# Performance work log

Hardware: AMD Instinct MI355X
Metric: run time of the kernel (lower is better)

Reference implementation:

```python
import jax, jax.numpy as jnp
import numpy as np

IN_SIZE = 1024
OUT_SIZE = 3 * IN_SIZE  # must equal 3*in_size for trigger_a * attn broadcast
B, S = 32, 512


def setup_inputs() -> dict:
    key = jax.random.key(0)
    ks = jax.random.split(key, 8)
    h_state = jax.random.normal(ks[0], (B, S, 2 * IN_SIZE), dtype=jnp.float32)
    x = jax.random.normal(ks[1], (B, S, IN_SIZE), dtype=jnp.float32)
    trigger = jax.random.randint(ks[2], (B,), 0, S)
    mask = jax.random.randint(ks[3], (B, S), 0, 2).astype(jnp.int32)
    # learned params (nn.Linear: y = x @ W.T + b; store pre-transposed as (in, out))
    Wa = jax.random.normal(ks[4], (3 * IN_SIZE, OUT_SIZE), dtype=jnp.float32) / np.sqrt(3 * IN_SIZE)
    ba = jnp.zeros((OUT_SIZE,), dtype=jnp.float32)
    Ws = jax.random.normal(ks[5], (2 * IN_SIZE, OUT_SIZE), dtype=jnp.float32) / np.sqrt(2 * IN_SIZE)
    bs = jnp.zeros((OUT_SIZE,), dtype=jnp.float32)
    return {"h_state": h_state, "x": x, "trigger": trigger, "mask": mask,
            "Wa": Wa, "ba": ba, "Ws": Ws, "bs": bs}


def reference(h_state, x, trigger, mask, Wa, ba, Ws, bs):
    # a: (B, S, 3*in_size)
    a = jnp.concatenate([h_state, x], axis=-1)
    b = a.shape[0]
    # one_hot + masked_select in the original == gather of the trigger row per batch
    trigger_a = a[jnp.arange(b), trigger]  # (B, 3*in_size)
    s = h_state.sum(axis=1)  # (B, 2*in_size)
    # et: (B, S, out_size)
    et = jnp.tanh(a @ Wa + ba + (s @ Ws + bs)[:, None, :])
    # masked_fill where mask == 0 (mask broadcast over feature dim)
    et = jnp.where(mask[:, :, None] == 0, jnp.float32(-1e9), et)
    # softmax over the FEATURE dim (dim=-1), as in the original; dropout in eval mode is identity
    attn = jax.nn.softmax(et, axis=-1)
    # trigger-weighted reduction over the sequence dim
    out = (trigger_a[:, None, :] * attn).sum(axis=1)  # (B, out_size)
    return out
```

## Files before the change

kernel.cpp:

```cpp
#include <hip/hip_runtime.h>
#include <hip/hip_bf16.h>
#include <hip/hip_fp16.h>


namespace {
constexpr int SIN  = 1024;
constexpr int KH   = 2048;
constexpr int NF   = 3072;
constexpr int NBAT = 32;
constexpr int NS   = 512;
constexpr int NM   = NBAT * NS;
constexpr int NDB  = NF / 64;
constexpr int KC   = 8;
constexpr int NKT  = NF / 64;
}

typedef unsigned short u16;
typedef __bf16 bf16x8 __attribute__((ext_vector_type(8)));
typedef float  f32x4  __attribute__((ext_vector_type(4)));

#define ASYNC_CP16(gptr, lptr)                                                              \
  __builtin_amdgcn_global_load_lds((__attribute__((address_space(1))) void*)(gptr),         \
                                   (__attribute__((address_space(3))) void*)(lptr), 16, 0, 0)

__device__ __forceinline__ u16 f2b(float f) {
  union { float f; unsigned u; } v; v.f = f;
  unsigned u = v.u;
  u += 0x7FFFu + ((u >> 16) & 1u);
  return (u16)(u >> 16);
}

__global__ __launch_bounds__(64) void k_cnt(const int* __restrict__ mask,
                                            int* __restrict__ bcnt) {
  int b = blockIdx.x, t = threadIdx.x;
  int c = 0;
#pragma unroll
  for (int i = 0; i < NS / 64; ++i) c += mask[b * NS + i * 64 + t];
#pragma unroll
  for (int off = 32; off >= 1; off >>= 1) c += __shfl_down(c, off, 64);
  if (t == 0) bcnt[b] = c;
}

__global__ __launch_bounds__(64) void k_scan(const int* __restrict__ bcnt,
                                             int* __restrict__ boff,
                                             int* __restrict__ meta) {
  if (threadIdx.x == 0) {
    int run = 0;
    for (int b = 0; b < NBAT; ++b) { boff[b] = run; run += bcnt[b]; }
    meta[0] = run;
    meta[1] = (run + 255) & ~255;
  }
}

__global__ __launch_bounds__(512) void k_gather(const int* __restrict__ mask,
                                                const int* __restrict__ boff,
                                                const int* __restrict__ meta,
                                                int* __restrict__ rowmap) {
  __shared__ int ps[NS];
  int b = blockIdx.x, t = threadIdx.x;
  int m = mask[b * NS + t];
  ps[t] = m;
  __syncthreads();
#pragma unroll
  for (int off = 1; off < NS; off <<= 1) {
    int v = (t >= off) ? ps[t - off] : 0;
    __syncthreads();
    ps[t] += v;
    __syncthreads();
  }
  if (m) rowmap[boff[b] + ps[t] - m] = b * NS + t;
  if (b == 0) {
    int Mc = meta[0], McPad = meta[1];
    if (Mc + t < McPad) rowmap[Mc + t] = 0;
  }
}

__global__ __launch_bounds__(256) void k_sum_h(const float* __restrict__ h,
                                               float* __restrict__ s) {
  int b = blockIdx.x;
  int d = blockIdx.y * 256 + threadIdx.x;
  const float* p = h + (size_t)b * NS * KH + d;
  float acc = 0.f;
#pragma unroll 8
  for (int t = 0; t < NS; ++t) acc += p[(size_t)t * KH];
  s[b * KH + d] = acc;
}

__global__ __launch_bounds__(256) void k_base1(const float* __restrict__ s,
                                               const float* __restrict__ Ws,
                                               float* __restrict__ basep) {
  __shared__ float sT[NBAT][KH / KC];
  int f  = blockIdx.x * 256 + threadIdx.x;
  int k0 = blockIdx.y * (KH / KC);
  for (int it = 0; it < NBAT; ++it) {
    int idx = it * 256 + threadIdx.x;
    int b = idx >> 8, kk = idx & 255;
    sT[b][kk] = s[b * KH + k0 + kk];
  }
  __syncthreads();
  float acc[NBAT] = {};
  for (int k = 0; k < KH / KC; ++k) {
    float w = Ws[(size_t)(k0 + k) * NF + f];
#pragma unroll
    for (int b = 0; b < NBAT; ++b) acc[b] += sT[b][k] * w;
  }
#pragma unroll
  for (int b = 0; b < NBAT; ++b)
    basep[((size_t)blockIdx.y * NBAT + b) * NF + f] = acc[b];
}

__global__ __launch_bounds__(256) void k_base2(const float* __restrict__ basep,
                                               const float* __restrict__ ba,
                                               const float* __restrict__ bs,
                                               float* __restrict__ base) {
  int b = blockIdx.x;
  int f = blockIdx.y * 256 + threadIdx.x;
  float acc = 0.f;
#pragma unroll
  for (int kc = 0; kc < KC; ++kc) acc += basep[((size_t)kc * NBAT + b) * NF + f];
  base[b * NF + f] = acc + ba[f] + bs[f];
}

__global__ __launch_bounds__(256) void k_cvt_a(const float* __restrict__ h,
                                               const float* __restrict__ x,
                                               const int* __restrict__ rowmap,
                                               const int* __restrict__ meta,
                                               u16* __restrict__ A) {
  int tid = blockIdx.x * 256 + threadIdx.x;
  int i = tid / (NF / 4);
  if (i >= meta[1]) return;
  int k = (tid - i * (NF / 4)) * 4;
  ushort4 o;
  if (i >= meta[0]) {
    o.x = o.y = o.z = o.w = 0;
  } else {
    int ro = rowmap[i];
    int b = ro >> 9, t = ro & 511;
    const float* src = (k < KH) ? h + ((size_t)b * NS + t) * KH + k
                                : x + ((size_t)b * NS + t) * SIN + (k - KH);
    float4 v = *(const float4*)src;
    o.x = f2b(v.x); o.y = f2b(v.y); o.z = f2b(v.z); o.w = f2b(v.w);
  }
  *(ushort4*)(A + (size_t)i * NF + k) = o;
}

__global__ __launch_bounds__(256) void k_wat(const float* __restrict__ Wa,
                                             u16* __restrict__ WaT) {
  __shared__ float tile[64][65];
  int k0 = blockIdx.x * 64, f0 = blockIdx.y * 64;
  int tid = threadIdx.x;
  int col4 = (tid & 15) * 4, row = tid >> 4;
#pragma unroll
  for (int rr = 0; rr < 64; rr += 16) {
    float4 v = *(const float4*)(Wa + (size_t)(k0 + row + rr) * NF + f0 + col4);
    tile[row + rr][col4 + 0] = v.x; tile[row + rr][col4 + 1] = v.y;
    tile[row + rr][col4 + 2] = v.z; tile[row + rr][col4 + 3] = v.w;
  }
  __syncthreads();
#pragma unroll
  for (int rr = 0; rr < 64; rr += 16) {
    int f = f0 + row + rr;
    ushort4 o;
    o.x = f2b(tile[col4 + 0][row + rr]); o.y = f2b(tile[col4 + 1][row + rr]);
    o.z = f2b(tile[col4 + 2][row + rr]); o.w = f2b(tile[col4 + 3][row + rr]);
    *(ushort4*)(WaT + (size_t)f * NF + k0 + col4) = o;
  }
}

#define LDSOFF(row, gg) ((row) * 32 + ((((gg) ^ (((row) >> 1) & 3))) << 3))

#define LDB4(BUF, KS)                                                        \
  _Pragma("unroll") for (int nf = 0; nf < 4; ++nf) {                         \
    int rb = wc * 64 + nf * 16 + lr;                                         \
    bfr[nf] = *(const bf16x8*)&lds[BUF][1][KS][LDSOFF(rb, g)];               \
  }

#define LDA4(BUF, KS, MH)                                                    \
  _Pragma("unroll") for (int mf = 0; mf < 4; ++mf) {                         \
    int ra = wr * 128 + ((MH) * 4 + mf) * 16 + lr;                           \
    afr[mf] = *(const bf16x8*)&lds[BUF][0][KS][LDSOFF(ra, g)];               \
  }

#define MFMA16(MH)                                                           \
  _Pragma("unroll") for (int mf = 0; mf < 4; ++mf)                           \
  _Pragma("unroll") for (int nf = 0; nf < 4; ++nf)                           \
    acc[(MH) * 4 + mf][nf] = __builtin_amdgcn_mfma_f32_16x16x32_bf16(        \
        afr[mf], bfr[nf], acc[(MH) * 4 + mf][nf], 0, 0, 0);

#define STAGE(SMAT, SBUF, SKS, SKT)                                          \
  if ((SKT) < NKT) {                                                         \
    _Pragma("unroll") for (int q = 0; q < 2; ++q) {                          \
      const u16* src = ((SMAT) ? pB[q] : pA[q]) + (SKT) * 64 + (SKS) * 32;   \
      ASYNC_CP16(src, &lds[SBUF][SMAT][SKS][q * 4096 + wid * 512]);          \
    }                                                                        \
  }

#define PH(BUF, KS, MH, SMAT, SBUF, SKS, SKT, VM)                            \
  {                                                                          \
    if ((MH) == 0) { LDB4(BUF, KS) }                                         \
    LDA4(BUF, KS, MH)                                                        \
    STAGE(SMAT, SBUF, SKS, SKT)                                              \
    __builtin_amdgcn_s_barrier();                                            \
    asm volatile("s_waitcnt lgkmcnt(0)" ::: "memory");                       \
    __builtin_amdgcn_s_setprio(1);                                           \
    MFMA16(MH)                                                               \
    __builtin_amdgcn_s_setprio(0);                                           \
    if (VM) asm volatile("s_waitcnt vmcnt(4)" ::: "memory");                 \
    __builtin_amdgcn_s_barrier();                                            \
  }

__global__ __launch_bounds__(512, 2) void k_gemm(const u16* __restrict__ A,
                                                 const u16* __restrict__ Wt,
                                                 const float* __restrict__ base,
                                                 const int* __restrict__ rowmap,
                                                 const int* __restrict__ meta,
                                                 __half* __restrict__ P,
                                                 float* __restrict__ Dpart) {
  __shared__ __align__(16) u16 lds[2][2][2][8192];
  const int MT   = meta[1] >> 8;
  const int nact = MT * 12;
  const int flat = blockIdx.x;
  if (flat >= nact) return;
  const int qx = nact >> 3, rx = nact & 7;
  const int xcd = flat & 7, idx = flat >> 3;
  const int swz = (xcd < rx) ? xcd * (qx + 1) + idx
                             : rx * (qx + 1) + (xcd - rx) * qx + idx;
  const int mt = swz / 12, nt = swz - mt * 12;
  const int r0 = mt << 8, c0 = nt << 8;

  const int tid = threadIdx.x;
  const int wid = tid >> 6, lane = tid & 63;
  const int wr = wid >> 2, wc = wid & 3;
  const int g = lane >> 4, lr = lane & 15;

  const u16* pA[2]; const u16* pB[2];
#pragma unroll
  for (int q = 0; q < 2; ++q) {
    int c = q * 512 + tid;
    int row = c >> 2;
    int kc8 = (((c & 3) ^ ((row >> 1) & 3)) << 3);
    pA[q] = A  + (size_t)(r0 + row) * NF + kc8;
    pB[q] = Wt + (size_t)(c0 + row) * NF + kc8;
  }

  f32x4 acc[8][4] = {};
  bf16x8 afr[4], bfr[4];

  STAGE(0, 0, 0, 0) STAGE(1, 0, 0, 0)
  STAGE(0, 0, 1, 0) STAGE(1, 0, 1, 0)
  STAGE(0, 1, 0, 1) STAGE(1, 1, 0, 1)
  asm volatile("s_waitcnt vmcnt(4)" ::: "memory");
  __builtin_amdgcn_s_barrier();

#pragma unroll 1
  for (int i = 0; i < NKT / 2; ++i) {
    const int kt1 = 2 * i + 1, kt2 = 2 * i + 2, kt3 = 2 * i + 3;
    PH(0, 0, 0, 0, 1, 1, kt1, 0)
    PH(0, 0, 1, 1, 1, 1, kt1, 0)
    PH(0, 1, 0, 0, 0, 0, kt2, 0)
    PH(0, 1, 1, 1, 0, 0, kt2, 1)
    PH(1, 0, 0, 0, 0, 1, kt2, 0)
    PH(1, 0, 1, 1, 0, 1, kt2, 0)
    PH(1, 1, 0, 0, 1, 0, kt3, 0)
    PH(1, 1, 1, 1, 1, 0, kt3, 1)
  }

  const int cbase = c0 + wc * 64;
#pragma unroll
  for (int mf = 0; mf < 8; ++mf) {
#pragma unroll
    for (int j = 0; j < 4; ++j) {
      int i = r0 + wr * 128 + mf * 16 + g * 4 + j;
      int b = rowmap[i] >> 9;
      float rs = 0.f;
#pragma unroll
      for (int nf = 0; nf < 4; ++nf) {
        int ccn = cbase + nf * 16 + lr;
        float z  = acc[mf][nf][j] + base[b * NF + ccn];
        z        = fminf(fmaxf(z, -15.f), 15.f);
        float e2 = __expf(2.f * z);
        float th = (e2 - 1.f) / (e2 + 1.f);
        float p  = __expf(th);
        P[(size_t)i * NF + ccn] = __float2half(p);
        rs += p;
      }
#pragma unroll
      for (int off = 1; off < 16; off <<= 1) rs += __shfl_xor(rs, off, 64);
      if (lr == 0) Dpart[(size_t)i * NDB + (cbase >> 6)] = rs;
    }
  }
}

__global__ __launch_bounds__(256) void k_invd(const float* __restrict__ Dpart,
                                              const int* __restrict__ meta,
                                              float* __restrict__ invD) {
  int i = blockIdx.x * 256 + threadIdx.x;
  if (i >= meta[1]) return;
  float d = 0.f;
#pragma unroll
  for (int q = 0; q < NDB; ++q) d += Dpart[(size_t)i * NDB + q];
  invD[i] = 1.0f / d;
}

__global__ __launch_bounds__(384) void k_final(const __half* __restrict__ P,
                                               const float* __restrict__ invD,
                                               const int* __restrict__ boff,
                                               const int* __restrict__ bcnt,
                                               const float* __restrict__ h,
                                               const float* __restrict__ x,
                                               const int* __restrict__ trig,
                                               float* __restrict__ out) {
  int b = blockIdx.x;
  int f0 = threadIdx.x * 8;
  int off = boff[b], cnt = bcnt[b];
  const __half* Pp = P + (size_t)off * NF + f0;
  const float*  iv = invD + off;
  float acc[8] = {};
  for (int t = 0; t < cnt; ++t) {
    int4 v = *(const int4*)(Pp + (size_t)t * NF);
    float ivt = iv[t];
    const __half2* h2 = (const __half2*)&v;
#pragma unroll
    for (int k = 0; k < 4; ++k) {
      float2 f2 = __half22float2(h2[k]);
      acc[2 * k]     += f2.x * ivt;
      acc[2 * k + 1] += f2.y * ivt;
    }
  }
  float uni = (float)(NS - cnt) * (1.0f / (float)NF);
  int tr = trig[b];
#pragma unroll
  for (int k = 0; k < 8; ++k) {
    int f = f0 + k;
    float ta = (f < KH) ? h[((size_t)b * NS + tr) * KH + f]
                        : x[((size_t)b * NS + tr) * SIN + f - KH];
    out[b * NF + f] = (acc[k] + uni) * ta;
  }
}

extern "C" void kernel_launch(void* const* d_in, const int* in_sizes, int n_in,
                              void* d_out, int out_size, void* d_ws, size_t ws_size,
                              hipStream_t stream) {
  const float* h_state = (const float*)d_in[0];
  const float* x       = (const float*)d_in[1];
  const int*   trigger = (const int*)d_in[2];
  const int*   mask    = (const int*)d_in[3];
  const float* Wa      = (const float*)d_in[4];
  const float* ba      = (const float*)d_in[5];
  const float* Ws      = (const float*)d_in[6];
  const float* bs      = (const float*)d_in[7];
  float*       out     = (float*)d_out;

  char* w = (char*)d_ws;
  u16*    Abf   = (u16*)w;                 w += (size_t)NM * NF * 2;
  u16*    WaT   = (u16*)w;                 w += (size_t)NF * NF * 2;
  __half* P     = (__half*)w;              w += (size_t)NM * NF * 2;
  float*  s     = (float*)w;               w += (size_t)NBAT * KH * 4;
  float*  base  = (float*)w;               w += (size_t)NBAT * NF * 4;
  float*  Dpart = (float*)w;               w += (size_t)NM * NDB * 4;
  float*  basep = (float*)Dpart;
  float*  invD  = (float*)w;               w += (size_t)NM * 4;
  int*    rowmap= (int*)w;                 w += (size_t)NM * 4;
  int*    bcnt  = (int*)w;                 w += 128;
  int*    boff  = (int*)w;                 w += 128;
  int*    meta  = (int*)w;                 w += 128;

  (void)in_sizes; (void)n_in; (void)out_size; (void)ws_size;

  k_cnt   <<<dim3(NBAT), 64, 0, stream>>>(mask, bcnt);
  k_scan  <<<dim3(1), 64, 0, stream>>>(bcnt, boff, meta);
  k_gather<<<dim3(NBAT), 512, 0, stream>>>(mask, boff, meta, rowmap);
  k_sum_h <<<dim3(NBAT, KH / 256), 256, 0, stream>>>(h_state, s);
  k_cvt_a <<<dim3(NM * (NF / 4) / 256), 256, 0, stream>>>(h_state, x, rowmap, meta, Abf);
  k_wat   <<<dim3(NF / 64, NF / 64), 256, 0, stream>>>(Wa, WaT);
  k_base1 <<<dim3(NF / 256, KC), 256, 0, stream>>>(s, Ws, basep);
  k_base2 <<<dim3(NBAT, NF / 256), 256, 0, stream>>>(basep, ba, bs, base);
  k_gemm  <<<dim3((NF / 256) * (NM / 256)), 512, 0, stream>>>(Abf, WaT, base, rowmap, meta, P, Dpart);
  k_invd  <<<dim3(NM / 256), 256, 0, stream>>>(Dpart, meta, invD);
  k_final <<<dim3(NBAT), 384, 0, stream>>>(P, invD, boff, bcnt, h_state, x, trigger, out);
}
```

Measured before the change: 464.8 us.

## Split final reduction across sequence chunks and relax GEMM vmcnt waits

The final weighted sum over the sequence, which ran as only 32 blocks, becomes a two-stage reduction. The first stage uses 8 sequence chunks per batch across feature tiles and writes partial sums into a reused workspace; the second stage sums the partials and applies the trigger scaling. Separately, the GEMM pipeline drops the conditional vmcnt(4) waits and waits on vmcnt(6) in every phase, with vmcnt(8) in the prologue, to keep more async loads in flight. The wait change risks a race if the count no longer covers the stage about to be read. The first reduction stage also uses scalar half loads, which are less efficient than the previous vectorized loads.

```diff
diff --git a/kernel.cpp b/kernel.cpp
--- a/kernel.cpp
+++ b/kernel.cpp
@@ -13,6 +13,7 @@
 constexpr int NDB  = NF / 64;
 constexpr int KC   = 8;
 constexpr int NKT  = NF / 64;
+constexpr int NCH  = 8;
 }
 
 typedef unsigned short u16;
@@ -195,7 +196,7 @@
     }                                                                        \
   }
 
-#define PH(BUF, KS, MH, SMAT, SBUF, SKS, SKT, VM)                            \
+#define PH(BUF, KS, MH, SMAT, SBUF, SKS, SKT)                                \
   {                                                                          \
     if ((MH) == 0) { LDB4(BUF, KS) }                                         \
     LDA4(BUF, KS, MH)                                                        \
@@ -205,7 +206,7 @@
     __builtin_amdgcn_s_setprio(1);                                           \
     MFMA16(MH)                                                               \
     __builtin_amdgcn_s_setprio(0);                                           \
-    if (VM) asm volatile("s_waitcnt vmcnt(4)" ::: "memory");                 \
+    asm volatile("s_waitcnt vmcnt(6)" ::: "memory");                         \
     __builtin_amdgcn_s_barrier();                                            \
   }
 
@@ -249,20 +250,20 @@
   STAGE(0, 0, 0, 0) STAGE(1, 0, 0, 0)
   STAGE(0, 0, 1, 0) STAGE(1, 0, 1, 0)
   STAGE(0, 1, 0, 1) STAGE(1, 1, 0, 1)
-  asm volatile("s_waitcnt vmcnt(4)" ::: "memory");
+  asm volatile("s_waitcnt vmcnt(8)" ::: "memory");
   __builtin_amdgcn_s_barrier();
 
 #pragma unroll 1
   for (int i = 0; i < NKT / 2; ++i) {
     const int kt1 = 2 * i + 1, kt2 = 2 * i + 2, kt3 = 2 * i + 3;
-    PH(0, 0, 0, 0, 1, 1, kt1, 0)
-    PH(0, 0, 1, 1, 1, 1, kt1, 0)
-    PH(0, 1, 0, 0, 0, 0, kt2, 0)
-    PH(0, 1, 1, 1, 0, 0, kt2, 1)
-    PH(1, 0, 0, 0, 0, 1, kt2, 0)
-    PH(1, 0, 1, 1, 0, 1, kt2, 0)
-    PH(1, 1, 0, 0, 1, 0, kt3, 0)
-    PH(1, 1, 1, 1, 1, 0, kt3, 1)
+    PH(0, 0, 0, 0, 1, 1, kt1)
+    PH(0, 0, 1, 1, 1, 1, kt1)
+    PH(0, 1, 0, 0, 0, 0, kt2)
+    PH(0, 1, 1, 1, 0, 0, kt2)
+    PH(1, 0, 0, 0, 0, 1, kt2)
+    PH(1, 0, 1, 1, 0, 1, kt2)
+    PH(1, 1, 0, 0, 1, 0, kt3)
+    PH(1, 1, 1, 1, 1, 0, kt3)
   }
 
   const int cbase = c0 + wc * 64;
@@ -302,40 +303,39 @@
   invD[i] = 1.0f / d;
 }
 
-__global__ __launch_bounds__(384) void k_final(const __half* __restrict__ P,
-                                               const float* __restrict__ invD,
-                                               const int* __restrict__ boff,
-                                               const int* __restrict__ bcnt,
-                                               const float* __restrict__ h,
-                                               const float* __restrict__ x,
-                                               const int* __restrict__ trig,
-                                               float* __restrict__ out) {
+__global__ __launch_bounds__(256) void k_final1(const __half* __restrict__ P,
+                                                const float* __restrict__ invD,
+                                                const int* __restrict__ boff,
+                                                const int* __restrict__ bcnt,
+                                                float* __restrict__ pb) {
+  int c = blockIdx.x;
+  int b = c >> 3, j = c & 7;
+  int f = blockIdx.y * 256 + threadIdx.x;
+  int cnt = bcnt[b];
+  int lo = j * 64, hi = min(cnt, lo + 64);
+  int off = boff[b];
+  float acc = 0.f;
+  for (int t = lo; t < hi; ++t)
+    acc += __half2float(P[(size_t)(off + t) * NF + f]) * invD[off + t];
+  pb[(size_t)c * NF + f] = acc;
+}
+
+__global__ __launch_bounds__(256) void k_final2(const float* __restrict__ pb,
+                                                const int* __restrict__ bcnt,
+                                                const float* __restrict__ h,
+                                                const float* __restrict__ x,
+                                                const int* __restrict__ trig,
+                                                float* __restrict__ out) {
   int b = blockIdx.x;
-  int f0 = threadIdx.x * 8;
-  int off = boff[b], cnt = bcnt[b];
-  const __half* Pp = P + (size_t)off * NF + f0;
-  const float*  iv = invD + off;
-  float acc[8] = {};
-  for (int t = 0; t < cnt; ++t) {
-    int4 v = *(const int4*)(Pp + (size_t)t * NF);
-    float ivt = iv[t];
-    const __half2* h2 = (const __half2*)&v;
-#pragma unroll
-    for (int k = 0; k < 4; ++k) {
-      float2 f2 = __half22float2(h2[k]);
-      acc[2 * k]     += f2.x * ivt;
-      acc[2 * k + 1] += f2.y * ivt;
-    }
-  }
-  float uni = (float)(NS - cnt) * (1.0f / (float)NF);
+  int f = blockIdx.y * 256 + threadIdx.x;
+  float acc = 0.f;
+#pragma unroll
+  for (int j = 0; j < NCH; ++j) acc += pb[(size_t)(b * NCH + j) * NF + f];
+  acc += (float)(NS - bcnt[b]) * (1.0f / (float)NF);
   int tr = trig[b];
-#pragma unroll
-  for (int k = 0; k < 8; ++k) {
-    int f = f0 + k;
-    float ta = (f < KH) ? h[((size_t)b * NS + tr) * KH + f]
-                        : x[((size_t)b * NS + tr) * SIN + f - KH];
-    out[b * NF + f] = (acc[k] + uni) * ta;
-  }
+  float ta = (f < KH) ? h[((size_t)b * NS + tr) * KH + f]
+                      : x[((size_t)b * NS + tr) * SIN + f - KH];
+  out[b * NF + f] = acc * ta;
 }
 
 extern "C" void kernel_launch(void* const* d_in, const int* in_sizes, int n_in,
@@ -359,6 +359,7 @@
   float*  base  = (float*)w;               w += (size_t)NBAT * NF * 4;
   float*  Dpart = (float*)w;               w += (size_t)NM * NDB * 4;
   float*  basep = (float*)Dpart;
+  float*  pb    = (float*)Dpart;
   float*  invD  = (float*)w;               w += (size_t)NM * 4;
   int*    rowmap= (int*)w;                 w += (size_t)NM * 4;
   int*    bcnt  = (int*)w;                 w += 128;
@@ -377,5 +378,6 @@
   k_base2 <<<dim3(NBAT, NF / 256), 256, 0, stream>>>(basep, ba, bs, base);
   k_gemm  <<<dim3((NF / 256) * (NM / 256)), 512, 0, stream>>>(Abf, WaT, base, rowmap, meta, P, Dpart);
   k_invd  <<<dim3(NM / 256), 256, 0, stream>>>(Dpart, meta, invD);
-  k_final <<<dim3(NBAT), 384, 0, stream>>>(P, invD, boff, bcnt, h_state, x, trigger, out);
-}
+  k_final1<<<dim3(NBAT * NCH, NF / 256), 256, 0, stream>>>(P, invD, boff, bcnt, pb);
+  k_final2<<<dim3(NBAT, NF / 256), 256, 0, stream>>>(pb, bcnt, h_state, x, trigger, out);
+}
```

Measured after the change: 423.0 us. 1.1x faster.
